# Performance work log

Hardware: AMD Instinct MI355X
Metric: run time of the kernel (lower is better)

## Reference

```python
import jax, jax.numpy as jnp
import numpy as np
import math

B, S, E, H = 4, 1024, 1024, 16
DH = E // H  # head dim = 64


def setup_inputs() -> dict:
    key = jax.random.key(0)
    ks = jax.random.split(key, 10)
    w_scale = math.sqrt(2.0 / (E + 3 * E))  # xavier-ish
    return {
        "x_real": jax.random.normal(ks[0], (B, S, E), jnp.float32),
        "x_imag": jax.random.normal(ks[1], (B, S, E), jnp.float32),
        "w_packed_real": jax.random.normal(ks[2], (3 * E, E), jnp.float32) * w_scale,
        "w_packed_imag": jax.random.normal(ks[3], (3 * E, E), jnp.float32) * w_scale,
        "b_packed_real": jax.random.normal(ks[4], (1, 3 * E), jnp.float32) * 0.02,
        "b_packed_imag": jax.random.normal(ks[5], (1, 3 * E), jnp.float32) * 0.02,
        "w_out_real": jax.random.normal(ks[6], (E, E), jnp.float32) * w_scale,
        "w_out_imag": jax.random.normal(ks[7], (E, E), jnp.float32) * w_scale,
        "b_out_real": jax.random.normal(ks[8], (1, E), jnp.float32) * 0.02,
        "b_out_imag": jax.random.normal(ks[9], (1, E), jnp.float32) * 0.02,
    }


def _to_c(r, i):
    return jax.lax.complex(r, i)


def _cmha(x, w_packed, b_packed, w_out, b_out):
    # packed QKV projection: x [B,S,E] @ W^T [E,3E] + b
    qkv = jnp.matmul(x, w_packed.T) + b_packed  # [B,S,3E]
    q, k, v = jnp.split(qkv, 3, axis=-1)  # each [B,S,E]
    # split heads -> [B,H,S,DH]
    split = lambda t: t.reshape(B, S, H, DH).transpose(0, 2, 1, 3)
    q, k, v = split(q), split(k), split(v)
    scale = 1.0 / math.sqrt(DH)
    scores = jnp.einsum("bhqd,bhkd->bhqk", q, k) * scale  # complex [B,H,S,S]
    # complex softmax: softmax over real and imag parts independently
    attn = jax.lax.complex(jax.nn.softmax(scores.real, axis=-1),
                           jax.nn.softmax(scores.imag, axis=-1))
    out = jnp.einsum("bhqk,bhkd->bhqd", attn, v)  # [B,H,S,DH]
    out = out.transpose(0, 2, 1, 3).reshape(B, S, E)
    return jnp.matmul(out, w_out.T) + b_out  # [B,S,E] complex


def reference(x_real, x_imag, w_packed_real, w_packed_imag, b_packed_real,
              b_packed_imag, w_out_real, w_out_imag, b_out_real, b_out_imag):
    x = _to_c(x_real, x_imag)
    w_packed = _to_c(w_packed_real, w_packed_imag)
    b_packed = _to_c(b_packed_real, b_packed_imag)
    w_out = _to_c(w_out_real, w_out_imag)
    b_out = _to_c(b_out_real, b_out_imag)
    return _cmha(x, w_packed, b_packed, w_out, b_out)
```

## Files before the change

kernel.cpp:

```cpp
#include <hip/hip_runtime.h>


typedef _Float16 f16;
typedef _Float16 f16x8 __attribute__((ext_vector_type(8)));
typedef _Float16 f16x4 __attribute__((ext_vector_type(4)));
typedef float f32x4 __attribute__((ext_vector_type(4)));
typedef float f32x16 __attribute__((ext_vector_type(16)));

#define MFMA16(a, b, c) __builtin_amdgcn_mfma_f32_16x16x32_f16(a, b, c, 0, 0, 0)
#define MFMA32(a, b, c) __builtin_amdgcn_mfma_f32_32x32x16_f16(a, b, c, 0, 0, 0)

__device__ inline void load_lds16(const void* g, void* l) {
  __builtin_amdgcn_global_load_lds(
      (const __attribute__((address_space(1))) unsigned int*)g,
      (__attribute__((address_space(3))) unsigned int*)l, 16, 0, 0);
}

__device__ inline unsigned pkrtz(float a, float b) {
  auto t = __builtin_amdgcn_cvt_pkrtz(a, b);
  return __builtin_bit_cast(unsigned, t);
}


__global__ void pack_x_kernel(const float* __restrict__ xr, const float* __restrict__ xi,
                              f16* __restrict__ XC) {
  int i = blockIdx.x * 256 + threadIdx.x;
  if (i >= (4096 * 2048 / 4)) return;
  int idx = i * 4;
  int m = idx >> 11, k = idx & 2047;
  const float* src = (k < 1024) ? (xr + (size_t)m * 1024 + k) : (xi + (size_t)m * 1024 + k - 1024);
  float4 v = *(const float4*)src;
  f16x4 o = {(f16)v.x, (f16)v.y, (f16)v.z, (f16)v.w};
  *(f16x4*)(XC + idx) = o;
}

__global__ void pack_wqkv_kernel(const float* __restrict__ wr, const float* __restrict__ wi,
                                 f16* __restrict__ W) {
  int i = blockIdx.x * 256 + threadIdx.x;
  if (i >= (3072 * 2048 / 4)) return;
  int idx = i * 4;
  int n = idx >> 11, k = idx & 2047;
  const float* base;
  float sgn = 1.f;
  if (k < 1024) base = wr + (size_t)n * 1024 + k;
  else { base = wi + (size_t)n * 1024 + k - 1024; sgn = -1.f; }
  float4 v = *(const float4*)base;
  f16x4 o = {(f16)(sgn * v.x), (f16)(sgn * v.y), (f16)(sgn * v.z), (f16)(sgn * v.w)};
  *(f16x4*)(W + idx) = o;
}

__global__ void pack_wout_kernel(const float* __restrict__ wor, const float* __restrict__ woi,
                                 f16* __restrict__ W) {
  int i = blockIdx.x * 256 + threadIdx.x;
  if (i >= (2048 * 2048 / 4)) return;
  int idx = i * 4;
  int n = idx >> 11, k = idx & 2047;
  const float* base;
  float sgn = 1.f;
  if (n < 1024) {
    if (k < 1024) base = wor + (size_t)n * 1024 + k;
    else { base = woi + (size_t)n * 1024 + k - 1024; sgn = -1.f; }
  } else {
    int n2 = n - 1024;
    if (k < 1024) base = woi + (size_t)n2 * 1024 + k;
    else base = wor + (size_t)n2 * 1024 + k - 1024;
  }
  float4 v = *(const float4*)base;
  f16x4 o = {(f16)(sgn * v.x), (f16)(sgn * v.y), (f16)(sgn * v.z), (f16)(sgn * v.w)};
  *(f16x4*)(W + idx) = o;
}

struct GemmParams {
  f16 *QC, *KCr, *KCi, *VCT;
  const float *bpr, *bpi;
  float* out;
  const float *bor, *boi;
  int out_complex;
};


__global__ __launch_bounds__(256, 3) void gemm1_kernel(const f16* __restrict__ A,
                                                       const f16* __restrict__ B,
                                                       GemmParams p) {
  const int KW = 2048;
  __shared__ alignas(16) f16 sAr[2][4096];
  __shared__ alignas(16) f16 sAi[2][4096];
  __shared__ alignas(16) f16 sBr[2][2048];
  __shared__ alignas(16) f16 sBu[2][2048];
  const int tid = threadIdx.x;
  const int w = tid >> 6, l = tid & 63;
  const int lr = l & 15, lk = l >> 4;
  const int lin = blockIdx.x;
  const int xcd = lin & 7, idx = lin >> 3;
  const int mt = idx / 6, ntl = idx % 6;
  const int tm0 = mt * 128;
  const int tn0 = (xcd * 6 + ntl) * 64;
  const int wm = (w >> 1) * 64, wn = (w & 1) * 32;

  const int srow = tid >> 2;
  const int sk8 = ((tid & 3) ^ ((tid >> 3) & 3)) * 8;
  const f16* gAr = A + (size_t)(tm0 + srow) * KW + sk8;
  const f16* gAi = A + (size_t)(tm0 + srow) * KW + 1024 + sk8;
  const f16* gBr = B + (size_t)(tn0 + srow) * KW + sk8;
  const f16* gBu = B + (size_t)(tn0 + srow) * KW + 1024 + sk8;
  const int dst = w * 512;

#define STG(buf, k0) do {                                                  \
    load_lds16(gAr + (size_t)(k0), &sAr[buf][dst]);                        \
    load_lds16(gAr + (size_t)64 * KW + (size_t)(k0), &sAr[buf][2048 + dst]);\
    load_lds16(gAi + (size_t)(k0), &sAi[buf][dst]);                        \
    load_lds16(gAi + (size_t)64 * KW + (size_t)(k0), &sAi[buf][2048 + dst]);\
    load_lds16(gBr + (size_t)(k0), &sBr[buf][dst]);                        \
    load_lds16(gBu + (size_t)(k0), &sBu[buf][dst]);                        \
  } while (0)

  f32x4 a1[4][2] = {};
  f32x4 aU[4][2] = {};
  f32x4 a3[4][2] = {};

  STG(0, 0);
  asm volatile("s_waitcnt vmcnt(0)" ::: "memory");
  __syncthreads();

  const int ca = (lk ^ ((lr >> 1) & 3)) * 8;

  for (int t = 0; t < 32; ++t) {
    const int buf = t & 1;
    if (t < 31) STG(buf ^ 1, (t + 1) * 32);
    f16x8 ar[4], ai[4], br[2], bu[2];
#pragma unroll
    for (int mi = 0; mi < 4; ++mi) {
      ar[mi] = *(const f16x8*)&sAr[buf][(wm + mi * 16 + lr) * 32 + ca];
      ai[mi] = *(const f16x8*)&sAi[buf][(wm + mi * 16 + lr) * 32 + ca];
    }
#pragma unroll
    for (int nj = 0; nj < 2; ++nj) {
      br[nj] = *(const f16x8*)&sBr[buf][(wn + nj * 16 + lr) * 32 + ca];
      bu[nj] = *(const f16x8*)&sBu[buf][(wn + nj * 16 + lr) * 32 + ca];
    }
#pragma unroll
    for (int mi = 0; mi < 4; ++mi)
#pragma unroll
      for (int nj = 0; nj < 2; ++nj) {
        a1[mi][nj] = MFMA16(ar[mi], br[nj], a1[mi][nj]);
        aU[mi][nj] = MFMA16(ai[mi], bu[nj], aU[mi][nj]);
      }
#pragma unroll
    for (int mi = 0; mi < 4; ++mi) ar[mi] = ar[mi] + ai[mi];
#pragma unroll
    for (int nj = 0; nj < 2; ++nj) br[nj] = br[nj] - bu[nj];
#pragma unroll
    for (int mi = 0; mi < 4; ++mi)
#pragma unroll
      for (int nj = 0; nj < 2; ++nj)
        a3[mi][nj] = MFMA16(ar[mi], br[nj], a3[mi][nj]);
    asm volatile("s_waitcnt vmcnt(0)" ::: "memory");
    __syncthreads();
  }
#undef STG

#pragma unroll
  for (int mi = 0; mi < 4; ++mi)
#pragma unroll
    for (int nj = 0; nj < 2; ++nj) {
      int n = tn0 + wn + nj * 16 + lr;
      float br_ = p.bpr[n], bi_ = p.bpi[n];
      int part = n >> 10;
      int e = n & 1023, h = e >> 6, dd = e & 63;
      int m0 = tm0 + wm + mi * 16 + lk * 4;
      int bb = m0 >> 10, s0 = m0 & 1023;
      size_t bh = (size_t)bb * 16 + h;
      f32x4 re = a1[mi][nj] + aU[mi][nj];
      f32x4 im = a3[mi][nj] - a1[mi][nj] + aU[mi][nj];
      if (part == 0) {
#pragma unroll
        for (int r = 0; r < 4; ++r) {
          size_t o = (bh * 1024 + s0 + r) * 128;
          p.QC[o + dd] = (f16)((re[r] + br_) * 0.125f);
          p.QC[o + 64 + dd] = (f16)((im[r] + bi_) * 0.125f);
        }
      } else if (part == 1) {
#pragma unroll
        for (int r = 0; r < 4; ++r) {
          float vr = re[r] + br_, vi = im[r] + bi_;
          size_t o = (bh * 1024 + s0 + r) * 128;
          p.KCr[o + dd] = (f16)vr; p.KCr[o + 64 + dd] = (f16)(-vi);
          p.KCi[o + dd] = (f16)vi; p.KCi[o + 64 + dd] = (f16)vr;
        }
      } else {
        f16x4 vvr, vvi;
#pragma unroll
        for (int r = 0; r < 4; ++r) { vvr[r] = (f16)(re[r] + br_); vvi[r] = (f16)(im[r] + bi_); }
        *(f16x4*)&p.VCT[((bh * 128 + dd)) * 1024 + s0] = vvr;
        *(f16x4*)&p.VCT[((bh * 128 + 64 + dd)) * 1024 + s0] = vvi;
      }
    }
}


__global__ __launch_bounds__(256) void gemm_out_kernel(const f16* __restrict__ A,
                                                       const f16* __restrict__ B,
                                                       GemmParams p) {
  const int K = 2048;
  __shared__ alignas(16) f16 sA[128 * 64];
  __shared__ alignas(16) f16 sB[128 * 64];
  const int tid = threadIdx.x;
  const int w = tid >> 6, l = tid & 63;
  const int lr = l & 15, lk = l >> 4;
  const int nwg = gridDim.x * gridDim.y;
  const int lin = blockIdx.y * gridDim.x + blockIdx.x;
  const int qq = nwg >> 3, rr = nwg & 7;
  const int xcd = lin & 7, off = lin >> 3;
  const int swz = (xcd < rr ? xcd * (qq + 1) : rr * (qq + 1) + (xcd - rr) * qq) + off;
  const int tm0 = (swz / gridDim.x) * 128;
  const int tn0 = (swz % gridDim.x) * 128;
  const int wm = (w >> 1) * 64, wn = (w & 1) * 64;

  f32x4 acc[4][4] = {};

  for (int k0 = 0; k0 < K; k0 += 64) {
#pragma unroll
    for (int i = 0; i < 4; ++i) {
      int slot = i * 256 + tid;
      int row = slot >> 3;
      int cg = (slot & 7) ^ (row & 7);
      load_lds16(A + (size_t)(tm0 + row) * K + k0 + cg * 8, &sA[(size_t)(i * 256 + (w << 6)) * 8]);
      load_lds16(B + (size_t)(tn0 + row) * K + k0 + cg * 8, &sB[(size_t)(i * 256 + (w << 6)) * 8]);
    }
    __syncthreads();
#pragma unroll
    for (int kk = 0; kk < 2; ++kk) {
      f16x8 af[4], bf[4];
#pragma unroll
      for (int t = 0; t < 4; ++t) {
        int rowA = wm + t * 16 + lr;
        af[t] = *(const f16x8*)&sA[rowA * 64 + ((kk * 4 + lk) ^ (rowA & 7)) * 8];
        int rowB = wn + t * 16 + lr;
        bf[t] = *(const f16x8*)&sB[rowB * 64 + ((kk * 4 + lk) ^ (rowB & 7)) * 8];
      }
#pragma unroll
      for (int mt = 0; mt < 4; ++mt)
#pragma unroll
        for (int nt = 0; nt < 4; ++nt) acc[mt][nt] = MFMA16(af[mt], bf[nt], acc[mt][nt]);
    }
    __syncthreads();
  }

#pragma unroll
  for (int mt = 0; mt < 4; ++mt)
#pragma unroll
    for (int nt = 0; nt < 4; ++nt)
#pragma unroll
      for (int r = 0; r < 4; ++r) {
        int m = tm0 + wm + mt * 16 + lk * 4 + r;
        int n = tn0 + wn + nt * 16 + lr;
        float val = acc[mt][nt][r];
        if (n < 1024) {
          float v2 = val + p.bor[n];
          if (p.out_complex) p.out[((size_t)m * 1024 + n) * 2] = v2;
          else p.out[(size_t)m * 1024 + n] = v2;
        } else {
          if (p.out_complex) p.out[((size_t)m * 1024 + n - 1024) * 2 + 1] = val + p.boi[n - 1024];
        }
      }
}


__global__ __launch_bounds__(256, 2) void attn_kernel(const f16* __restrict__ QC,
                                                      const f16* __restrict__ KCr,
                                                      const f16* __restrict__ KCi,
                                                      const f16* __restrict__ VCT,
                                                      f16* __restrict__ OC) {
  __shared__ alignas(16) f16 sKr[2][32 * 128];
  __shared__ alignas(16) f16 sKi[2][32 * 128];
  __shared__ alignas(16) f16 sV[2][128 * 32];
  const int tid = threadIdx.x;
  const int w = tid >> 6, l = tid & 63;
  const int lq = l & 31, hi = l >> 5;
  const int bid = blockIdx.x;
  const int xx = bid & 7, yy = bid >> 3;
  const int bh = xx + ((yy >> 3) << 3);
  const int qt = yy & 7;
  const int q0 = qt * 128 + w * 32;
  const f16* Qb = QC + (size_t)bh * 1024 * 128;
  const f16* Krb = KCr + (size_t)bh * 1024 * 128;
  const f16* Kib = KCi + (size_t)bh * 1024 * 128;
  const f16* Vb = VCT + (size_t)bh * 128 * 1024;

  f16x8 qf[8];
#pragma unroll
  for (int c = 0; c < 8; ++c)
    qf[c] = *(const f16x8*)&Qb[(size_t)(q0 + lq) * 128 + c * 16 + hi * 8];

  f32x16 accR[4] = {};
  f32x16 accI[4] = {};
  float m_r = -1e30f, l_r = 0.f, m_i = -1e30f, l_i = 0.f;

  const int sprow = tid >> 3;
  const int cK = (tid & 7) ^ ((tid >> 4) & 7);
  const f16* gKr = Krb + (size_t)(tid >> 4) * 128 + ((tid >> 3) & 1) * 64 + cK * 8;
  const f16* gKi = Kib + (size_t)(tid >> 4) * 128 + ((tid >> 3) & 1) * 64 + cK * 8;
  const int cV = (tid & 7) ^ (sprow & 7);
  const f16* gV = Vb + (size_t)(sprow * 2 + (cV >> 2)) * 1024 + (cV & 3) * 8;
  const int ldsW = w * 512;

#define STAGE(s, k0)                                                      \
  do {                                                                    \
    load_lds16(gKr + (size_t)(k0) * 128, &sKr[s][ldsW]);                  \
    load_lds16(gKr + (size_t)(k0) * 128 + 16 * 128, &sKr[s][2048 + ldsW]);\
    load_lds16(gKi + (size_t)(k0) * 128, &sKi[s][ldsW]);                  \
    load_lds16(gKi + (size_t)(k0) * 128 + 16 * 128, &sKi[s][2048 + ldsW]);\
    load_lds16(gV + (size_t)(k0), &sV[s][ldsW]);                          \
    load_lds16(gV + (size_t)64 * 1024 + (size_t)(k0), &sV[s][2048 + ldsW]);\
  } while (0)

  STAGE(0, 0);
  asm volatile("s_waitcnt vmcnt(0)" ::: "memory");
  __syncthreads();
  int cur = 0;

  for (int t = 0; t < 32; ++t) {
    if (t < 31) STAGE(cur ^ 1, (t + 1) * 32);

    f32x16 sr = {}, si = {};
    __builtin_amdgcn_s_setprio(1);
#pragma unroll
    for (int c = 0; c < 8; ++c) {
      int fc = c * 2 + hi;
      int prow = lq * 2 + (fc >> 3);
      int swzc = (fc & 7) ^ (lq & 7);
      f16x8 kr = *(const f16x8*)&sKr[cur][prow * 64 + swzc * 8];
      f16x8 ki = *(const f16x8*)&sKi[cur][prow * 64 + swzc * 8];
      sr = MFMA32(kr, qf[c], sr);
      si = MFMA32(ki, qf[c], si);
    }
    __builtin_amdgcn_s_setprio(0);

    f16x8 prf[2], pif[2];
#pragma unroll
    for (int part = 0; part < 2; ++part) {
      const f32x16& s = part ? si : sr;
      float& m = part ? m_i : m_r;
      float& lsum = part ? l_i : l_r;
      f32x16* acc = part ? accI : accR;
      float vm = s[0];
#pragma unroll
      for (int j = 1; j < 16; ++j) vm = fmaxf(vm, s[j]);
      vm = fmaxf(vm, __shfl_xor(vm, 32));
      if (__any(vm > m + 8.f)) {
        float mn = fmaxf(m, vm);
        float sc = __expf(m - mn);
        lsum *= sc;
#pragma unroll
        for (int a = 0; a < 4; ++a)
#pragma unroll
          for (int j = 0; j < 16; ++j) acc[a][j] *= sc;
        m = mn;
      }
      float p[16];
      float ls = 0.f;
#pragma unroll
      for (int j = 0; j < 16; ++j) { p[j] = __expf(s[j] - m); ls += p[j]; }
      lsum += ls;
      unsigned a0 = pkrtz(p[0], p[1]), b0 = pkrtz(p[4], p[5]);
      unsigned a1 = pkrtz(p[2], p[3]), b1 = pkrtz(p[6], p[7]);
      unsigned a2 = pkrtz(p[8], p[9]), b2 = pkrtz(p[12], p[13]);
      unsigned a3 = pkrtz(p[10], p[11]), b3 = pkrtz(p[14], p[15]);
      asm("v_permlane32_swap_b32 %0, %1" : "+v"(a0), "+v"(b0));
      asm("v_permlane32_swap_b32 %0, %1" : "+v"(a1), "+v"(b1));
      asm("v_permlane32_swap_b32 %0, %1" : "+v"(a2), "+v"(b2));
      asm("v_permlane32_swap_b32 %0, %1" : "+v"(a3), "+v"(b3));
      union { unsigned u[4]; f16x8 v; } f0, f1;
      f0.u[0] = a0; f0.u[1] = a1; f0.u[2] = b0; f0.u[3] = b1;
      f1.u[0] = a2; f1.u[1] = a3; f1.u[2] = b2; f1.u[3] = b3;
      if (part) { pif[0] = f0.v; pif[1] = f1.v; }
      else      { prf[0] = f0.v; prf[1] = f1.v; }
    }

    __builtin_amdgcn_s_setprio(1);
#pragma unroll
    for (int ft = 0; ft < 4; ++ft) {
#pragma unroll
      for (int ks = 0; ks < 2; ++ks) {
        int feat = ft * 32 + lq;
        int prow = feat >> 1;
        int swzc = (((feat & 1) * 4 + ks * 2 + hi) ^ (prow & 7));
        f16x8 vf = *(const f16x8*)&sV[cur][prow * 64 + swzc * 8];
        accR[ft] = MFMA32(vf, prf[ks], accR[ft]);
        accI[ft] = MFMA32(vf, pif[ks], accI[ft]);
      }
    }
    __builtin_amdgcn_s_setprio(0);

    asm volatile("s_waitcnt vmcnt(0)" ::: "memory");
    __syncthreads();
    cur ^= 1;
  }
#undef STAGE

  float lr = l_r + __shfl_xor(l_r, 32);
  float li = l_i + __shfl_xor(l_i, 32);
  float ilr = 1.f / lr, ili = 1.f / li;
  const int bb = bh >> 4, h = bh & 15;
  const int q = q0 + lq;
  f16* rowp = OC + ((size_t)bb * 1024 + q) * 2048 + h * 64;
#pragma unroll
  for (int tt = 0; tt < 2; ++tt) {
#pragma unroll
    for (int g = 0; g < 4; ++g) {
      int d0 = tt * 32 + g * 8 + hi * 4;
      f16x4 ov, oiv;
#pragma unroll
      for (int j = 0; j < 4; ++j) {
        int rg = g * 4 + j;
        float orv = accR[tt][rg] * ilr - accI[tt + 2][rg] * ili;
        float oivv = accR[tt + 2][rg] * ilr + accI[tt][rg] * ili;
        ov[j] = (f16)orv;
        oiv[j] = (f16)oivv;
      }
      *(f16x4*)(rowp + d0) = ov;
      *(f16x4*)(rowp + 1024 + d0) = oiv;
    }
  }
}


extern "C" void kernel_launch(void* const* d_in, const int* in_sizes, int n_in,
                              void* d_out, int out_size, void* d_ws, size_t ws_size,
                              hipStream_t stream) {
  const float* xr = (const float*)d_in[0];
  const float* xi = (const float*)d_in[1];
  const float* wpr = (const float*)d_in[2];
  const float* wpi = (const float*)d_in[3];
  const float* bpr = (const float*)d_in[4];
  const float* bpi = (const float*)d_in[5];
  const float* wor = (const float*)d_in[6];
  const float* woi = (const float*)d_in[7];
  const float* bor = (const float*)d_in[8];
  const float* boi = (const float*)d_in[9];

  f16* ws = (f16*)d_ws;
  f16* XC = ws;
  f16* WQKV = XC + 8388608;
  f16* QC = WQKV + 6291456;
  f16* KCr = QC + 8388608;
  f16* KCi = KCr + 8388608;
  f16* VCT = KCi + 8388608;
  f16* OC = VCT + 8388608;
  f16* WOUT = OC + 8388608;

  pack_x_kernel<<<8192, 256, 0, stream>>>(xr, xi, XC);
  pack_wqkv_kernel<<<6144, 256, 0, stream>>>(wpr, wpi, WQKV);
  pack_wout_kernel<<<4096, 256, 0, stream>>>(wor, woi, WOUT);

  GemmParams p1 = {};
  p1.QC = QC; p1.KCr = KCr; p1.KCi = KCi; p1.VCT = VCT;
  p1.bpr = bpr; p1.bpi = bpi;
  gemm1_kernel<<<1536, 256, 0, stream>>>(XC, WQKV, p1);

  attn_kernel<<<512, 256, 0, stream>>>(QC, KCr, KCi, VCT, OC);

  GemmParams p2 = {};
  p2.out = (float*)d_out; p2.bor = bor; p2.boi = boi;
  p2.out_complex = (out_size == 8388608) ? 1 : 0;
  int ntilesN = p2.out_complex ? 16 : 8;
  gemm_out_kernel<<<dim3(ntilesN, 32), 256, 0, stream>>>(OC, WOUT, p2);
}
```

Before: 263.3 us.

## Apply 3-multiply complex trick to QK^T and output GEMM, shrink K storage

The attention score step now uses a Gauss/Karatsuba 3-MFMA complex product (qr·kr, qi·ki, (qr+qi)·(kr+ki)) in place of two MFMAs over doubled-width packed K. K is stored as separate real and imaginary 64-wide arrays, which halves K global traffic and LDS usage. The output projection reuses the templated 3-multiply gemm kernel instead of a separate real-embedded 2048-wide GEMM, so its weight packing shrinks to 1024 rows. This cuts MFMA work and memory traffic but adds f16 sum rounding error and extra vector adds inside the attention loop.

New measurement: 268.7 us. 1.02x slower.

```diff
diff --git a/kernel.cpp b/kernel.cpp
--- a/kernel.cpp
+++ b/kernel.cpp
@@ -34,10 +34,10 @@
   *(f16x4*)(XC + idx) = o;
 }
 
-__global__ void pack_wqkv_kernel(const float* __restrict__ wr, const float* __restrict__ wi,
-                                 f16* __restrict__ W) {
+__global__ void pack_w_kernel(const float* __restrict__ wr, const float* __restrict__ wi,
+                              f16* __restrict__ W, int rows) {
   int i = blockIdx.x * 256 + threadIdx.x;
-  if (i >= (3072 * 2048 / 4)) return;
+  if (i >= (rows * 2048 / 4)) return;
   int idx = i * 4;
   int n = idx >> 11, k = idx & 2047;
   const float* base;
@@ -49,29 +49,8 @@
   *(f16x4*)(W + idx) = o;
 }
 
-__global__ void pack_wout_kernel(const float* __restrict__ wor, const float* __restrict__ woi,
-                                 f16* __restrict__ W) {
-  int i = blockIdx.x * 256 + threadIdx.x;
-  if (i >= (2048 * 2048 / 4)) return;
-  int idx = i * 4;
-  int n = idx >> 11, k = idx & 2047;
-  const float* base;
-  float sgn = 1.f;
-  if (n < 1024) {
-    if (k < 1024) base = wor + (size_t)n * 1024 + k;
-    else { base = woi + (size_t)n * 1024 + k - 1024; sgn = -1.f; }
-  } else {
-    int n2 = n - 1024;
-    if (k < 1024) base = woi + (size_t)n2 * 1024 + k;
-    else base = wor + (size_t)n2 * 1024 + k - 1024;
-  }
-  float4 v = *(const float4*)base;
-  f16x4 o = {(f16)(sgn * v.x), (f16)(sgn * v.y), (f16)(sgn * v.z), (f16)(sgn * v.w)};
-  *(f16x4*)(W + idx) = o;
-}
-
 struct GemmParams {
-  f16 *QC, *KCr, *KCi, *VCT;
+  f16 *QC, *KR, *KI, *VCT;
   const float *bpr, *bpi;
   float* out;
   const float *bor, *boi;
@@ -79,9 +58,10 @@
 };
 
 
-__global__ __launch_bounds__(256, 3) void gemm1_kernel(const f16* __restrict__ A,
-                                                       const f16* __restrict__ B,
-                                                       GemmParams p) {
+template <int MODE>
+__global__ __launch_bounds__(256, 3) void gemm_kernel(const f16* __restrict__ A,
+                                                      const f16* __restrict__ B,
+                                                      GemmParams p, int ntPerXcd) {
   const int KW = 2048;
   __shared__ alignas(16) f16 sAr[2][4096];
   __shared__ alignas(16) f16 sAi[2][4096];
@@ -92,9 +72,9 @@
   const int lr = l & 15, lk = l >> 4;
   const int lin = blockIdx.x;
   const int xcd = lin & 7, idx = lin >> 3;
-  const int mt = idx / 6, ntl = idx % 6;
+  const int mt = idx / ntPerXcd, ntl = idx % ntPerXcd;
   const int tm0 = mt * 128;
-  const int tn0 = (xcd * 6 + ntl) * 64;
+  const int tn0 = (xcd * ntPerXcd + ntl) * 64;
   const int wm = (w >> 1) * 64, wn = (w & 1) * 32;
 
   const int srow = tid >> 2;
@@ -164,116 +144,61 @@
 #pragma unroll
     for (int nj = 0; nj < 2; ++nj) {
       int n = tn0 + wn + nj * 16 + lr;
-      float br_ = p.bpr[n], bi_ = p.bpi[n];
-      int part = n >> 10;
-      int e = n & 1023, h = e >> 6, dd = e & 63;
       int m0 = tm0 + wm + mi * 16 + lk * 4;
-      int bb = m0 >> 10, s0 = m0 & 1023;
-      size_t bh = (size_t)bb * 16 + h;
       f32x4 re = a1[mi][nj] + aU[mi][nj];
       f32x4 im = a3[mi][nj] - a1[mi][nj] + aU[mi][nj];
-      if (part == 0) {
-#pragma unroll
-        for (int r = 0; r < 4; ++r) {
-          size_t o = (bh * 1024 + s0 + r) * 128;
-          p.QC[o + dd] = (f16)((re[r] + br_) * 0.125f);
-          p.QC[o + 64 + dd] = (f16)((im[r] + bi_) * 0.125f);
-        }
-      } else if (part == 1) {
-#pragma unroll
-        for (int r = 0; r < 4; ++r) {
-          float vr = re[r] + br_, vi = im[r] + bi_;
-          size_t o = (bh * 1024 + s0 + r) * 128;
-          p.KCr[o + dd] = (f16)vr; p.KCr[o + 64 + dd] = (f16)(-vi);
-          p.KCi[o + dd] = (f16)vi; p.KCi[o + 64 + dd] = (f16)vr;
+      if constexpr (MODE == 0) {
+        float br_ = p.bpr[n], bi_ = p.bpi[n];
+        int part = n >> 10;
+        int e = n & 1023, h = e >> 6, dd = e & 63;
+        int bb = m0 >> 10, s0 = m0 & 1023;
+        size_t bh = (size_t)bb * 16 + h;
+        if (part == 0) {
+#pragma unroll
+          for (int r = 0; r < 4; ++r) {
+            size_t o = (bh * 1024 + s0 + r) * 128;
+            p.QC[o + dd] = (f16)((re[r] + br_) * 0.125f);
+            p.QC[o + 64 + dd] = (f16)((im[r] + bi_) * 0.125f);
+          }
+        } else if (part == 1) {
+#pragma unroll
+          for (int r = 0; r < 4; ++r) {
+            size_t o = (bh * 1024 + s0 + r) * 64;
+            p.KR[o + dd] = (f16)(re[r] + br_);
+            p.KI[o + dd] = (f16)(im[r] + bi_);
+          }
+        } else {
+          f16x4 vvr, vvi;
+#pragma unroll
+          for (int r = 0; r < 4; ++r) { vvr[r] = (f16)(re[r] + br_); vvi[r] = (f16)(im[r] + bi_); }
+          *(f16x4*)&p.VCT[((bh * 128 + dd)) * 1024 + s0] = vvr;
+          *(f16x4*)&p.VCT[((bh * 128 + 64 + dd)) * 1024 + s0] = vvi;
         }
       } else {
-        f16x4 vvr, vvi;
-#pragma unroll
-        for (int r = 0; r < 4; ++r) { vvr[r] = (f16)(re[r] + br_); vvi[r] = (f16)(im[r] + bi_); }
-        *(f16x4*)&p.VCT[((bh * 128 + dd)) * 1024 + s0] = vvr;
-        *(f16x4*)&p.VCT[((bh * 128 + 64 + dd)) * 1024 + s0] = vvi;
-      }
-    }
-}
-
-
-__global__ __launch_bounds__(256) void gemm_out_kernel(const f16* __restrict__ A,
-                                                       const f16* __restrict__ B,
-                                                       GemmParams p) {
-  const int K = 2048;
-  __shared__ alignas(16) f16 sA[128 * 64];
-  __shared__ alignas(16) f16 sB[128 * 64];
-  const int tid = threadIdx.x;
-  const int w = tid >> 6, l = tid & 63;
-  const int lr = l & 15, lk = l >> 4;
-  const int nwg = gridDim.x * gridDim.y;
-  const int lin = blockIdx.y * gridDim.x + blockIdx.x;
-  const int qq = nwg >> 3, rr = nwg & 7;
-  const int xcd = lin & 7, off = lin >> 3;
-  const int swz = (xcd < rr ? xcd * (qq + 1) : rr * (qq + 1) + (xcd - rr) * qq) + off;
-  const int tm0 = (swz / gridDim.x) * 128;
-  const int tn0 = (swz % gridDim.x) * 128;
-  const int wm = (w >> 1) * 64, wn = (w & 1) * 64;
-
-  f32x4 acc[4][4] = {};
-
-  for (int k0 = 0; k0 < K; k0 += 64) {
-#pragma unroll
-    for (int i = 0; i < 4; ++i) {
-      int slot = i * 256 + tid;
-      int row = slot >> 3;
-      int cg = (slot & 7) ^ (row & 7);
-      load_lds16(A + (size_t)(tm0 + row) * K + k0 + cg * 8, &sA[(size_t)(i * 256 + (w << 6)) * 8]);
-      load_lds16(B + (size_t)(tn0 + row) * K + k0 + cg * 8, &sB[(size_t)(i * 256 + (w << 6)) * 8]);
-    }
-    __syncthreads();
-#pragma unroll
-    for (int kk = 0; kk < 2; ++kk) {
-      f16x8 af[4], bf[4];
-#pragma unroll
-      for (int t = 0; t < 4; ++t) {
-        int rowA = wm + t * 16 + lr;
-        af[t] = *(const f16x8*)&sA[rowA * 64 + ((kk * 4 + lk) ^ (rowA & 7)) * 8];
-        int rowB = wn + t * 16 + lr;
-        bf[t] = *(const f16x8*)&sB[rowB * 64 + ((kk * 4 + lk) ^ (rowB & 7)) * 8];
-      }
-#pragma unroll
-      for (int mt = 0; mt < 4; ++mt)
-#pragma unroll
-        for (int nt = 0; nt < 4; ++nt) acc[mt][nt] = MFMA16(af[mt], bf[nt], acc[mt][nt]);
-    }
-    __syncthreads();
-  }
-
-#pragma unroll
-  for (int mt = 0; mt < 4; ++mt)
-#pragma unroll
-    for (int nt = 0; nt < 4; ++nt)
-#pragma unroll
-      for (int r = 0; r < 4; ++r) {
-        int m = tm0 + wm + mt * 16 + lk * 4 + r;
-        int n = tn0 + wn + nt * 16 + lr;
-        float val = acc[mt][nt][r];
-        if (n < 1024) {
-          float v2 = val + p.bor[n];
-          if (p.out_complex) p.out[((size_t)m * 1024 + n) * 2] = v2;
-          else p.out[(size_t)m * 1024 + n] = v2;
-        } else {
-          if (p.out_complex) p.out[((size_t)m * 1024 + n - 1024) * 2 + 1] = val + p.boi[n - 1024];
+        float br_ = p.bor[n], bi_ = p.boi[n];
+#pragma unroll
+        for (int r = 0; r < 4; ++r) {
+          size_t m = (size_t)(m0 + r);
+          if (p.out_complex) {
+            p.out[(m * 1024 + n) * 2] = re[r] + br_;
+            p.out[(m * 1024 + n) * 2 + 1] = im[r] + bi_;
+          } else {
+            p.out[m * 1024 + n] = re[r] + br_;
+          }
         }
       }
+    }
 }
 
 
 __global__ __launch_bounds__(256, 2) void attn_kernel(const f16* __restrict__ QC,
-                                                      const f16* __restrict__ KCr,
-                                                      const f16* __restrict__ KCi,
+                                                      const f16* __restrict__ KR,
+                                                      const f16* __restrict__ KI,
                                                       const f16* __restrict__ VCT,
                                                       f16* __restrict__ OC) {
-  __shared__ alignas(16) f16 sKr[2][32 * 128];
-  __shared__ alignas(16) f16 sKi[2][32 * 128];
-  __shared__ alignas(16) f16 sV[2][128 * 32];
+  __shared__ alignas(16) f16 sKr[2][2048];
+  __shared__ alignas(16) f16 sKi[2][2048];
+  __shared__ alignas(16) f16 sV[2][4096];
   const int tid = threadIdx.x;
   const int w = tid >> 6, l = tid & 63;
   const int lq = l & 31, hi = l >> 5;
@@ -283,34 +208,36 @@
   const int qt = yy & 7;
   const int q0 = qt * 128 + w * 32;
   const f16* Qb = QC + (size_t)bh * 1024 * 128;
-  const f16* Krb = KCr + (size_t)bh * 1024 * 128;
-  const f16* Kib = KCi + (size_t)bh * 1024 * 128;
+  const f16* KRb = KR + (size_t)bh * 1024 * 64;
+  const f16* KIb = KI + (size_t)bh * 1024 * 64;
   const f16* Vb = VCT + (size_t)bh * 128 * 1024;
 
-  f16x8 qf[8];
-#pragma unroll
-  for (int c = 0; c < 8; ++c)
-    qf[c] = *(const f16x8*)&Qb[(size_t)(q0 + lq) * 128 + c * 16 + hi * 8];
+  f16x8 qr[4], qi[4], qs[4];
+#pragma unroll
+  for (int ks = 0; ks < 4; ++ks) {
+    qr[ks] = *(const f16x8*)&Qb[(size_t)(q0 + lq) * 128 + ks * 16 + hi * 8];
+    qi[ks] = *(const f16x8*)&Qb[(size_t)(q0 + lq) * 128 + 64 + ks * 16 + hi * 8];
+    qs[ks] = qr[ks] + qi[ks];
+  }
 
   f32x16 accR[4] = {};
   f32x16 accI[4] = {};
   float m_r = -1e30f, l_r = 0.f, m_i = -1e30f, l_i = 0.f;
 
+  const int srK = tid >> 3;
+  const int cgK = (tid & 7) ^ (srK & 7);
+  const f16* gKR = KRb + (size_t)srK * 64 + cgK * 8;
+  const f16* gKI = KIb + (size_t)srK * 64 + cgK * 8;
   const int sprow = tid >> 3;
-  const int cK = (tid & 7) ^ ((tid >> 4) & 7);
-  const f16* gKr = Krb + (size_t)(tid >> 4) * 128 + ((tid >> 3) & 1) * 64 + cK * 8;
-  const f16* gKi = Kib + (size_t)(tid >> 4) * 128 + ((tid >> 3) & 1) * 64 + cK * 8;
   const int cV = (tid & 7) ^ (sprow & 7);
   const f16* gV = Vb + (size_t)(sprow * 2 + (cV >> 2)) * 1024 + (cV & 3) * 8;
   const int ldsW = w * 512;
 
-#define STAGE(s, k0)                                                      \
-  do {                                                                    \
-    load_lds16(gKr + (size_t)(k0) * 128, &sKr[s][ldsW]);                  \
-    load_lds16(gKr + (size_t)(k0) * 128 + 16 * 128, &sKr[s][2048 + ldsW]);\
-    load_lds16(gKi + (size_t)(k0) * 128, &sKi[s][ldsW]);                  \
-    load_lds16(gKi + (size_t)(k0) * 128 + 16 * 128, &sKi[s][2048 + ldsW]);\
-    load_lds16(gV + (size_t)(k0), &sV[s][ldsW]);                          \
+#define STAGE(s, k0)                                                       \
+  do {                                                                     \
+    load_lds16(gKR + (size_t)(k0) * 64, &sKr[s][ldsW]);                    \
+    load_lds16(gKI + (size_t)(k0) * 64, &sKi[s][ldsW]);                    \
+    load_lds16(gV + (size_t)(k0), &sV[s][ldsW]);                           \
     load_lds16(gV + (size_t)64 * 1024 + (size_t)(k0), &sV[s][2048 + ldsW]);\
   } while (0)
 
@@ -322,24 +249,26 @@
   for (int t = 0; t < 32; ++t) {
     if (t < 31) STAGE(cur ^ 1, (t + 1) * 32);
 
-    f32x16 sr = {}, si = {};
+    f32x16 t1 = {}, uu = {}, t3 = {};
     __builtin_amdgcn_s_setprio(1);
 #pragma unroll
-    for (int c = 0; c < 8; ++c) {
-      int fc = c * 2 + hi;
-      int prow = lq * 2 + (fc >> 3);
-      int swzc = (fc & 7) ^ (lq & 7);
-      f16x8 kr = *(const f16x8*)&sKr[cur][prow * 64 + swzc * 8];
-      f16x8 ki = *(const f16x8*)&sKi[cur][prow * 64 + swzc * 8];
-      sr = MFMA32(kr, qf[c], sr);
-      si = MFMA32(ki, qf[c], si);
+    for (int ks = 0; ks < 4; ++ks) {
+      int ch = (((ks * 2 + hi) ^ (lq & 7))) * 8;
+      f16x8 kr = *(const f16x8*)&sKr[cur][lq * 64 + ch];
+      f16x8 ki = *(const f16x8*)&sKi[cur][lq * 64 + ch];
+      t1 = MFMA32(kr, qr[ks], t1);
+      uu = MFMA32(ki, qi[ks], uu);
+      f16x8 ksum = kr + ki;
+      t3 = MFMA32(ksum, qs[ks], t3);
     }
     __builtin_amdgcn_s_setprio(0);
+    t3 = t3 - t1 - uu;
+    t1 = t1 - uu;
 
     f16x8 prf[2], pif[2];
 #pragma unroll
     for (int part = 0; part < 2; ++part) {
-      const f32x16& s = part ? si : sr;
+      const f32x16& s = part ? t3 : t1;
       float& m = part ? m_i : m_r;
       float& lsum = part ? l_i : l_r;
       f32x16* acc = part ? accI : accR;
@@ -398,9 +327,9 @@
   }
 #undef STAGE
 
-  float lr = l_r + __shfl_xor(l_r, 32);
-  float li = l_i + __shfl_xor(l_i, 32);
-  float ilr = 1.f / lr, ili = 1.f / li;
+  float lr_ = l_r + __shfl_xor(l_r, 32);
+  float li_ = l_i + __shfl_xor(l_i, 32);
+  float ilr = 1.f / lr_, ili = 1.f / li_;
   const int bb = bh >> 4, h = bh & 15;
   const int q = q0 + lq;
   f16* rowp = OC + ((size_t)bb * 1024 + q) * 2048 + h * 64;
@@ -443,26 +372,25 @@
   f16* XC = ws;
   f16* WQKV = XC + 8388608;
   f16* QC = WQKV + 6291456;
-  f16* KCr = QC + 8388608;
-  f16* KCi = KCr + 8388608;
-  f16* VCT = KCi + 8388608;
+  f16* KR = QC + 8388608;
+  f16* KI = KR + 4194304;
+  f16* VCT = KI + 4194304;
   f16* OC = VCT + 8388608;
   f16* WOUT = OC + 8388608;
 
   pack_x_kernel<<<8192, 256, 0, stream>>>(xr, xi, XC);
-  pack_wqkv_kernel<<<6144, 256, 0, stream>>>(wpr, wpi, WQKV);
-  pack_wout_kernel<<<4096, 256, 0, stream>>>(wor, woi, WOUT);
+  pack_w_kernel<<<6144, 256, 0, stream>>>(wpr, wpi, WQKV, 3072);
+  pack_w_kernel<<<2048, 256, 0, stream>>>(wor, woi, WOUT, 1024);
 
   GemmParams p1 = {};
-  p1.QC = QC; p1.KCr = KCr; p1.KCi = KCi; p1.VCT = VCT;
+  p1.QC = QC; p1.KR = KR; p1.KI = KI; p1.VCT = VCT;
   p1.bpr = bpr; p1.bpi = bpi;
-  gemm1_kernel<<<1536, 256, 0, stream>>>(XC, WQKV, p1);
-
-  attn_kernel<<<512, 256, 0, stream>>>(QC, KCr, KCi, VCT, OC);
+  gemm_kernel<0><<<1536, 256, 0, stream>>>(XC, WQKV, p1, 6);
+
+  attn_kernel<<<512, 256, 0, stream>>>(QC, KR, KI, VCT, OC);
 
   GemmParams p2 = {};
   p2.out = (float*)d_out; p2.bor = bor; p2.boi = boi;
   p2.out_complex = (out_size == 8388608) ? 1 : 0;
-  int ntilesN = p2.out_complex ? 16 : 8;
-  gemm_out_kernel<<<dim3(ntilesN, 32), 256, 0, stream>>>(OC, WOUT, p2);
-}
+  gemm_kernel<1><<<512, 256, 0, stream>>>(OC, WOUT, p2, 2);
+}
```
